# Kernel tuning notes

Hardware: AMD Instinct MI355X
Metric: run time of the kernel (lower is better)

Reference implementation:

```python
import jax, jax.numpy as jnp
import numpy as np

EMBED_DIM = 1024
NUM_HEADS = 16
HEAD_DIM = EMBED_DIM // NUM_HEADS
SCALE = float(np.sqrt(HEAD_DIM))


def setup_inputs() -> dict:
    key = jax.random.key(0)
    ks = jax.random.split(key, 5)
    B, S, D = 4, 2048, EMBED_DIM
    lim_qkv = 1.0 / np.sqrt(D)
    lim_out = 1.0 / np.sqrt(D)
    return {
        "x": jax.random.normal(ks[0], (B, S, D), dtype=jnp.float32),
        "qkv_w": jax.random.uniform(ks[1], (3 * D, D), jnp.float32, -lim_qkv, lim_qkv),
        "qkv_b": jax.random.uniform(ks[2], (3 * D,), jnp.float32, -lim_qkv, lim_qkv),
        "out_w": jax.random.uniform(ks[3], (D, D), jnp.float32, -lim_out, lim_out),
        "out_b": jax.random.uniform(ks[4], (D,), jnp.float32, -lim_out, lim_out),
    }


def reference(x, qkv_w, qkv_b, out_w, out_b):
    B, S, D = x.shape
    H, Hd = NUM_HEADS, HEAD_DIM
    # qkv projection (torch Linear: x @ W.T + b)
    qkv = x @ qkv_w.T + qkv_b                      # [B, S, 3D]
    qkv = qkv.reshape(B, S, 3, H, Hd)
    q = jnp.transpose(qkv[:, :, 0], (0, 2, 1, 3))  # [B, H, S, Hd]
    k = jnp.transpose(qkv[:, :, 1], (0, 2, 1, 3))
    v = jnp.transpose(qkv[:, :, 2], (0, 2, 1, 3))
    attn = jnp.einsum("bhqd,bhkd->bhqk", q, k) / SCALE  # [B, H, S, S]
    attn = jax.nn.softmax(attn, axis=-1)
    out = jnp.einsum("bhqk,bhkd->bhqd", attn, v)        # [B, H, S, Hd]
    out = jnp.transpose(out, (0, 2, 1, 3)).reshape(B, S, D)
    return out @ out_w.T + out_b
```

## Files before the change

### kernel.cpp

```cpp
#include <hip/hip_runtime.h>

typedef unsigned short u16;
typedef __bf16 bf16x8 __attribute__((ext_vector_type(8)));
typedef __bf16 bf16x4 __attribute__((ext_vector_type(4)));
typedef float f32x4 __attribute__((ext_vector_type(4)));
typedef float f32x16 __attribute__((ext_vector_type(16)));
typedef unsigned u32x2 __attribute__((ext_vector_type(2)));

#define AS1 __attribute__((address_space(1)))
#define AS3 __attribute__((address_space(3)))

__device__ __forceinline__ void gload_lds16(const void* g, void* l) {
  __builtin_amdgcn_global_load_lds((const AS1 void*)g, (AS3 void*)l, 16, 0, 0);
}

__device__ __forceinline__ f32x4 mfma16(bf16x8 a, bf16x8 b, f32x4 c) {
  return __builtin_amdgcn_mfma_f32_16x16x32_bf16(a, b, c, 0, 0, 0);
}
__device__ __forceinline__ f32x16 mfma32(bf16x8 a, bf16x8 b, f32x16 c) {
  return __builtin_amdgcn_mfma_f32_32x32x16_bf16(a, b, c, 0, 0, 0);
}

#define QSCALE 0.18033688011112042f

__global__ __launch_bounds__(256) void k_cvt3(const float* __restrict__ s0, u16* __restrict__ d0, int n0,
                                              const float* __restrict__ s1, u16* __restrict__ d1, int n1,
                                              const float* __restrict__ s2, u16* __restrict__ d2, int n2) {
  int g = (blockIdx.x * 256 + threadIdx.x) * 8;
  const float* src;
  u16* dst;
  int i;
  if (g < n0) { src = s0; dst = d0; i = g; }
  else if (g < n0 + n1) { src = s1; dst = d1; i = g - n0; }
  else if (g < n0 + n1 + n2) { src = s2; dst = d2; i = g - n0 - n1; }
  else return;
  float4 a = *(const float4*)(src + i);
  float4 b = *(const float4*)(src + i + 4);
  union { bf16x8 v; uint4 q; } o;
  o.v[0] = (__bf16)a.x; o.v[1] = (__bf16)a.y; o.v[2] = (__bf16)a.z; o.v[3] = (__bf16)a.w;
  o.v[4] = (__bf16)b.x; o.v[5] = (__bf16)b.y; o.v[6] = (__bf16)b.z; o.v[7] = (__bf16)b.w;
  *(uint4*)(dst + i) = o.q;
}

template <int MODE, int BXN>
__global__ __launch_bounds__(512, 2) void k_gemm_big(
    const u16* __restrict__ A, const u16* __restrict__ W,
    const float* __restrict__ bias, float* __restrict__ Cout,
    u16* __restrict__ Qo, u16* __restrict__ Ko, u16* __restrict__ Vo) {
  __shared__ __align__(16) u16 LDS[2][6 * 4096];

  const int t = threadIdx.x;
  const int lane = t & 63;
  const int w = t >> 6;
  const int wm = w >> 1;
  const int wn = w & 1;
  const int lr = lane & 15;
  const int hi = lane >> 4;

  const int TOT = BXN * 32;
  const int flat = blockIdx.x;
  const int nb = (flat & 7) * (TOT >> 3) + (flat >> 3);
  const int by = nb / BXN;
  const int bx = nb - by * BXN;
  const int m0 = by * 256;
  const int n0 = bx * 128;

  const int tt = t & 255;
  const int g = t >> 8;
  const int tu = (tt & 15) ^ (tt >> 4);
  const int sro = (tu >> 3) * 32 + (tt >> 4);
  const int scol = (tu & 7) * 8;

  auto STAGE = [&](int buf, int kt, int pLo, int pHi) {
    for (int p = pLo; p < pHi; ++p) {
      int st = p * 2 + g;
      const u16* base = (st < 4) ? (A + (size_t)(m0 + st * 64) * 1024)
                                 : (W + (size_t)(n0 + (st - 4) * 64) * 1024);
#pragma unroll
      for (int i = 0; i < 2; ++i)
        gload_lds16(base + (size_t)(sro + i * 16) * 1024 + kt * 64 + scol,
                    &LDS[buf][st * 4096 + i * 2048 + tt * 8]);
    }
  };

  f32x4 acc[4][4] = {};

  STAGE(0, 0, 0, 3);

  for (int kt = 0; kt < 16; ++kt) {
    const int cur = kt & 1;
    asm volatile("s_waitcnt vmcnt(0)" ::: "memory");
    __builtin_amdgcn_sched_barrier(0);
    __builtin_amdgcn_s_barrier();
    __builtin_amdgcn_sched_barrier(0);

    const u16* ab = &LDS[cur][wm * 4096];
    const u16* bb = &LDS[cur][(4 + wn) * 4096];

#pragma unroll
    for (int ks = 0; ks < 2; ++ks) {
      bf16x8 af[4], bfr[4];
#pragma unroll
      for (int mi = 0; mi < 4; ++mi)
        af[mi] = *(const bf16x8*)(ab + ((mi & 1) * 16 + lr) * 128 +
                                  (((ks * 4 + hi + 8 * (mi >> 1)) ^ lr) << 3));
#pragma unroll
      for (int ni = 0; ni < 4; ++ni)
        bfr[ni] = *(const bf16x8*)(bb + ((ni & 1) * 16 + lr) * 128 +
                                   (((ks * 4 + hi + 8 * (ni >> 1)) ^ lr) << 3));
      if (kt + 1 < 16) STAGE(cur ^ 1, kt + 1, ks ? 2 : 0, ks ? 3 : 2);
      asm volatile("s_waitcnt lgkmcnt(0)" ::: "memory");
      __builtin_amdgcn_sched_barrier(0);
      __builtin_amdgcn_s_setprio(1);
#pragma unroll
      for (int mi = 0; mi < 4; ++mi)
#pragma unroll
        for (int ni = 0; ni < 4; ++ni)
          acc[mi][ni] = mfma16(bfr[ni], af[mi], acc[mi][ni]);
      __builtin_amdgcn_s_setprio(0);
      __builtin_amdgcn_sched_barrier(0);
      if (ks == 0) __builtin_amdgcn_s_barrier();
    }
  }

  f32x4 bv[4];
#pragma unroll
  for (int ni = 0; ni < 4; ++ni)
    bv[ni] = *(const f32x4*)(bias + n0 + wn * 64 + ni * 16 + hi * 4);

  if (MODE == 0) {
    const int N = BXN * 128;
#pragma unroll
    for (int mi = 0; mi < 4; ++mi) {
      const int m = m0 + wm * 64 + mi * 16 + lr;
#pragma unroll
      for (int ni = 0; ni < 4; ++ni) {
        f32x4 o = acc[mi][ni] + bv[ni];
        *(f32x4*)(Cout + (size_t)m * N + n0 + wn * 64 + ni * 16 + hi * 4) = o;
      }
    }
  } else {
    const int bb16 = m0 >> 11;
    const int sb = (m0 & 2047) + wm * 64;
    const int which = n0 >> 10;
    const int h = ((n0 & 1023) >> 6) + wn;

    if (which < 2) {
      const float scl = (which == 0) ? QSCALE : 1.0f;
      u16* dst = ((which == 0) ? Qo : Ko) + ((size_t)(bb16 * 16 + h) * 2048) * 64;
#pragma unroll
      for (int mi = 0; mi < 4; ++mi) {
        const int s = sb + mi * 16 + lr;
#pragma unroll
        for (int ni = 0; ni < 4; ++ni) {
          bf16x4 pk;
#pragma unroll
          for (int j = 0; j < 4; ++j)
            pk[j] = (__bf16)((acc[mi][ni][j] + bv[ni][j]) * scl);
          *(bf16x4*)(dst + (size_t)s * 64 + ni * 16 + hi * 4) = pk;
        }
      }
    } else {
      __syncthreads();
      u16* scr = &LDS[0][0] + w * 4608;
#pragma unroll
      for (int mi = 0; mi < 4; ++mi)
#pragma unroll
        for (int ni = 0; ni < 4; ++ni)
#pragma unroll
          for (int j = 0; j < 4; ++j) {
            union { __bf16 b; u16 u; } cv;
            cv.b = (__bf16)(acc[mi][ni][j] + bv[ni][j]);
            scr[(ni * 16 + hi * 4 + j) * 72 + mi * 16 + lr] = cv.u;
          }
      asm volatile("s_waitcnt lgkmcnt(0)" ::: "memory");
      __builtin_amdgcn_sched_barrier(0);
      u16* dst = Vo + ((size_t)((bb16 * 16 + h) * 64 + lane)) * 2048 + sb;
#pragma unroll
      for (int mc = 0; mc < 8; ++mc) {
        bf16x8 vv = *(const bf16x8*)(scr + lane * 72 + mc * 8);
        *(bf16x8*)(dst + mc * 8) = vv;
      }
    }
  }
}

__global__ __launch_bounds__(256, 4) void k_attn(const u16* __restrict__ Q,
                                                 const u16* __restrict__ K,
                                                 const u16* __restrict__ Vt,
                                                 u16* __restrict__ ctx) {
  __shared__ __align__(16) u16 Ks[2][64 * 64];
  __shared__ __align__(16) u16 Vs[2][64 * 64];

  const int t = threadIdx.x;
  const int lane = t & 63;
  const int w = t >> 6;
  const int r31 = lane & 31;
  const int hw = lane >> 5;

  const int bid = blockIdx.x;
  const int nb = (bid & 7) * 128 + (bid >> 3);
  const int bh = nb >> 4;
  const int q0 = (nb & 15) * 128;

  const u16* qp = Q + (size_t)bh * 2048 * 64;
  const u16* kp = K + (size_t)bh * 2048 * 64;
  const u16* vp = Vt + (size_t)bh * 64 * 2048;

  const int tu = (t & 15) ^ (t >> 4);
  const int srow = (tu >> 3) * 32 + (t >> 4);
  const int scol = (tu & 7) * 8;

#pragma unroll
  for (int i = 0; i < 2; i++)
    gload_lds16(kp + (size_t)(srow + i * 16) * 64 + scol, Ks[0] + i * 2048 + t * 8);
#pragma unroll
  for (int i = 0; i < 2; i++)
    gload_lds16(vp + (size_t)(srow + i * 16) * 2048 + scol, Vs[0] + i * 2048 + t * 8);

  bf16x8 aq[4];
  const u16* qrow = qp + (size_t)(q0 + w * 32 + r31) * 64 + hw * 8;
#pragma unroll
  for (int kd = 0; kd < 4; kd++) aq[kd] = *(const bf16x8*)(qrow + kd * 16);

  bf16x8 ones;
#pragma unroll
  for (int e = 0; e < 8; e++) ones[e] = (__bf16)1.0f;

  asm volatile("s_waitcnt vmcnt(0)" ::: "memory");
  __builtin_amdgcn_sched_barrier(0);
  __builtin_amdgcn_s_barrier();
  __builtin_amdgcn_sched_barrier(0);

  f32x16 o0 = {}, o1 = {}, l_acc = {};

  for (int kt = 0; kt < 32; kt++) {
    const int cur = kt & 1;
    if (kt + 1 < 32) {
      u16* kd_ = Ks[cur ^ 1];
      u16* vd_ = Vs[cur ^ 1];
#pragma unroll
      for (int i = 0; i < 2; i++)
        gload_lds16(kp + (size_t)((kt + 1) * 64 + srow + i * 16) * 64 + scol,
                    kd_ + i * 2048 + t * 8);
#pragma unroll
      for (int i = 0; i < 2; i++)
        gload_lds16(vp + (size_t)(srow + i * 16) * 2048 + (kt + 1) * 64 + scol,
                    vd_ + i * 2048 + t * 8);
      asm volatile("s_waitcnt vmcnt(4)" ::: "memory");
    } else {
      asm volatile("s_waitcnt vmcnt(0)" ::: "memory");
    }
    __builtin_amdgcn_sched_barrier(0);
    __builtin_amdgcn_s_barrier();
    __builtin_amdgcn_sched_barrier(0);

    const u16* kb = Ks[cur];
    const u16* vb = Vs[cur];

    f32x16 s0 = {}, s1 = {};
    __builtin_amdgcn_s_setprio(1);
#pragma unroll
    for (int kd = 0; kd < 4; kd++) {
      int sl0 = (((kd * 2 + hw) ^ (r31 & 15)) << 3);
      int sl1 = (((8 + kd * 2 + hw) ^ (r31 & 15)) << 3);
      bf16x8 ka0 = *(const bf16x8*)(kb + r31 * 128 + sl0);
      bf16x8 ka1 = *(const bf16x8*)(kb + r31 * 128 + sl1);
      s0 = mfma32(ka0, aq[kd], s0);
      s1 = mfma32(ka1, aq[kd], s1);
    }
    __builtin_amdgcn_s_setprio(0);

#pragma unroll
    for (int e = 0; e < 16; e++) {
      s0[e] = __builtin_amdgcn_exp2f(s0[e]);
      s1[e] = __builtin_amdgcn_exp2f(s1[e]);
    }

    __builtin_amdgcn_s_setprio(1);
#pragma unroll
    for (int tile = 0; tile < 2; tile++) {
      f32x16 st = tile ? s1 : s0;
      unsigned pk[8];
#pragma unroll
      for (int p = 0; p < 8; p++) {
        union { __bf16 h[2]; unsigned u; } cv;
        cv.h[0] = (__bf16)st[2 * p];
        cv.h[1] = (__bf16)st[2 * p + 1];
        pk[p] = cv.u;
      }
#pragma unroll
      for (int c = 0; c < 2; c++) {
        u32x2 ra = __builtin_amdgcn_permlane32_swap(pk[4 * c], pk[4 * c + 2], false, false);
        u32x2 rb = __builtin_amdgcn_permlane32_swap(pk[4 * c + 1], pk[4 * c + 3], false, false);
        union { unsigned u[4]; bf16x8 v; } pf;
        pf.u[0] = ra[0]; pf.u[1] = rb[0]; pf.u[2] = ra[1]; pf.u[3] = rb[1];
        const int kap = tile * 2 + c;
        int slv0 = (((kap * 2 + hw) ^ (r31 & 15)) << 3);
        int slv1 = (((8 + kap * 2 + hw) ^ (r31 & 15)) << 3);
        bf16x8 v0 = *(const bf16x8*)(vb + r31 * 128 + slv0);
        bf16x8 v1 = *(const bf16x8*)(vb + r31 * 128 + slv1);
        o0 = mfma32(v0, pf.v, o0);
        o1 = mfma32(v1, pf.v, o1);
        l_acc = mfma32(ones, pf.v, l_acc);
      }
    }
    __builtin_amdgcn_s_setprio(0);
    __builtin_amdgcn_sched_barrier(0);
    __builtin_amdgcn_s_barrier();
  }

  const int bb = bh >> 4, h = bh & 15;
  const float inv = 1.0f / l_acc[0];
  const size_t base = (size_t)(bb * 2048 + q0 + w * 32 + r31) * 1024 + h * 64;
#pragma unroll
  for (int g = 0; g < 4; g++) {
    bf16x4 p0, p1;
#pragma unroll
    for (int j = 0; j < 4; j++) {
      p0[j] = (__bf16)(o0[g * 4 + j] * inv);
      p1[j] = (__bf16)(o1[g * 4 + j] * inv);
    }
    *(bf16x4*)(ctx + base + g * 8 + hw * 4) = p0;
    *(bf16x4*)(ctx + base + 32 + g * 8 + hw * 4) = p1;
  }
}

extern "C" void kernel_launch(void* const* d_in, const int* in_sizes, int n_in,
                              void* d_out, int out_size, void* d_ws, size_t ws_size,
                              hipStream_t stream) {
  const float* x = (const float*)d_in[0];
  const float* qkv_w = (const float*)d_in[1];
  const float* qkv_b = (const float*)d_in[2];
  const float* out_w = (const float*)d_in[3];
  const float* out_b = (const float*)d_in[4];
  float* out = (float*)d_out;
  char* ws = (char*)d_ws;

  u16* xb    = (u16*)(ws + 0);
  u16* wqkvb = (u16*)(ws + 16777216);
  u16* wob   = (u16*)(ws + 23068672);
  u16* Qb    = (u16*)(ws + 25165824);
  u16* Kb    = (u16*)(ws + 41943040);
  u16* Vtb   = (u16*)(ws + 58720256);
  u16* ctx   = xb;

  k_cvt3<<<6144, 256, 0, stream>>>(x, xb, 8388608,
                                   qkv_w, wqkvb, 3145728,
                                   out_w, wob, 1048576);

  k_gemm_big<1, 24><<<768, 512, 0, stream>>>(xb, wqkvb, qkv_b, nullptr,
                                             Qb, Kb, Vtb);
  k_attn<<<1024, 256, 0, stream>>>(Qb, Kb, Vtb, ctx);
  k_gemm_big<0, 8><<<256, 512, 0, stream>>>(ctx, wob, out_b, out,
                                            nullptr, nullptr, nullptr);
}
```

Measured before the change: 198.6 us.

## Stagger KV tile order per block and use single barrier per iteration

Each block starts its key/value loop at a different tile offset (phase), so concurrently running blocks on the same head read different K/V tiles. The loop is restructured to wait on all outstanding loads and take one barrier at the top, then issue the next tile's prefetch, which drops the second barrier at the loop end. The first QK MFMA uses a constant zero accumulator instead of zero-initialised registers. The prefetch now overlaps only the current tile's compute rather than being issued ahead of the wait, and the fixed 32-tile wraparound assumes the sequence length.

After: 197.4 us. Within noise of the previous version (-0.6%).

```diff
diff --git a/kernel.cpp b/kernel.cpp
--- a/kernel.cpp
+++ b/kernel.cpp
@@ -202,6 +202,7 @@
   const int nb = (bid & 7) * 128 + (bid >> 3);
   const int bh = nb >> 4;
   const int q0 = (nb & 15) * 128;
+  const int phase = (((bid >> 8) ^ (bid >> 3)) & 3) * 8;
 
   const u16* qp = Q + (size_t)bh * 2048 * 64;
   const u16* kp = K + (size_t)bh * 2048 * 64;
@@ -213,10 +214,12 @@
 
 #pragma unroll
   for (int i = 0; i < 2; i++)
-    gload_lds16(kp + (size_t)(srow + i * 16) * 64 + scol, Ks[0] + i * 2048 + t * 8);
+    gload_lds16(kp + (size_t)(phase * 64 + srow + i * 16) * 64 + scol,
+                Ks[0] + i * 2048 + t * 8);
 #pragma unroll
   for (int i = 0; i < 2; i++)
-    gload_lds16(vp + (size_t)(srow + i * 16) * 2048 + scol, Vs[0] + i * 2048 + t * 8);
+    gload_lds16(vp + (size_t)(srow + i * 16) * 2048 + phase * 64 + scol,
+                Vs[0] + i * 2048 + t * 8);
 
   bf16x8 aq[4];
   const u16* qrow = qp + (size_t)(q0 + w * 32 + r31) * 64 + hw * 8;
@@ -226,42 +229,44 @@
   bf16x8 ones;
 #pragma unroll
   for (int e = 0; e < 8; e++) ones[e] = (__bf16)1.0f;
-
-  asm volatile("s_waitcnt vmcnt(0)" ::: "memory");
-  __builtin_amdgcn_sched_barrier(0);
-  __builtin_amdgcn_s_barrier();
-  __builtin_amdgcn_sched_barrier(0);
+  const f32x16 Z = {};
 
   f32x16 o0 = {}, o1 = {}, l_acc = {};
 
-  for (int kt = 0; kt < 32; kt++) {
-    const int cur = kt & 1;
-    if (kt + 1 < 32) {
-      u16* kd_ = Ks[cur ^ 1];
-      u16* vd_ = Vs[cur ^ 1];
-#pragma unroll
-      for (int i = 0; i < 2; i++)
-        gload_lds16(kp + (size_t)((kt + 1) * 64 + srow + i * 16) * 64 + scol,
-                    kd_ + i * 2048 + t * 8);
-#pragma unroll
-      for (int i = 0; i < 2; i++)
-        gload_lds16(vp + (size_t)(srow + i * 16) * 2048 + (kt + 1) * 64 + scol,
-                    vd_ + i * 2048 + t * 8);
-      asm volatile("s_waitcnt vmcnt(4)" ::: "memory");
-    } else {
-      asm volatile("s_waitcnt vmcnt(0)" ::: "memory");
-    }
+  for (int it = 0; it < 32; it++) {
+    const int cur = it & 1;
+    asm volatile("s_waitcnt vmcnt(0)" ::: "memory");
     __builtin_amdgcn_sched_barrier(0);
     __builtin_amdgcn_s_barrier();
     __builtin_amdgcn_sched_barrier(0);
 
+    if (it + 1 < 32) {
+      const int ktn = ((it + 1 + phase) & 31) * 64;
+      u16* kd_ = Ks[cur ^ 1];
+      u16* vd_ = Vs[cur ^ 1];
+#pragma unroll
+      for (int i = 0; i < 2; i++)
+        gload_lds16(kp + (size_t)(ktn + srow + i * 16) * 64 + scol,
+                    kd_ + i * 2048 + t * 8);
+#pragma unroll
+      for (int i = 0; i < 2; i++)
+        gload_lds16(vp + (size_t)(srow + i * 16) * 2048 + ktn + scol,
+                    vd_ + i * 2048 + t * 8);
+    }
+
     const u16* kb = Ks[cur];
     const u16* vb = Vs[cur];
 
-    f32x16 s0 = {}, s1 = {};
     __builtin_amdgcn_s_setprio(1);
-#pragma unroll
-    for (int kd = 0; kd < 4; kd++) {
+    f32x16 s0, s1;
+    {
+      bf16x8 ka0 = *(const bf16x8*)(kb + r31 * 128 + (((hw) ^ (r31 & 15)) << 3));
+      bf16x8 ka1 = *(const bf16x8*)(kb + r31 * 128 + (((8 + hw) ^ (r31 & 15)) << 3));
+      s0 = mfma32(ka0, aq[0], Z);
+      s1 = mfma32(ka1, aq[0], Z);
+    }
+#pragma unroll
+    for (int kd = 1; kd < 4; kd++) {
       int sl0 = (((kd * 2 + hw) ^ (r31 & 15)) << 3);
       int sl1 = (((8 + kd * 2 + hw) ^ (r31 & 15)) << 3);
       bf16x8 ka0 = *(const bf16x8*)(kb + r31 * 128 + sl0);
@@ -306,8 +311,6 @@
       }
     }
     __builtin_amdgcn_s_setprio(0);
-    __builtin_amdgcn_sched_barrier(0);
-    __builtin_amdgcn_s_barrier();
   }
 
   const int bb = bh >> 4, h = bh & 15;
```

## Software-pipeline attention loop: overlap QK/exp of next tile with PV of current

Applied to the files above, without the earlier changes.

Restructures the attention inner loop so the QK^T, exp and packing for key tile k+1 run in the same step as the P·V MMAs for tile k, with K and V staged into LDS at offset iterations. The row-sum is now computed with scalar adds and a cross-half shuffle instead of an extra MFMA against a ones vector. This aims to hide exp/pack latency behind matrix work and cut MFMA count, in exchange for more live registers and a full vmcnt(0) wait each sub-step.

Result: slower. 368.6 us (+85.6%).

```diff
diff --git a/kernel.cpp b/kernel.cpp
--- a/kernel.cpp
+++ b/kernel.cpp
@@ -19,6 +19,33 @@
 }
 __device__ __forceinline__ f32x16 mfma32(bf16x8 a, bf16x8 b, f32x16 c) {
   return __builtin_amdgcn_mfma_f32_32x32x16_bf16(a, b, c, 0, 0, 0);
+}
+
+__device__ __forceinline__ float rsum16(f32x16 v) {
+  float a0 = v[0] + v[1],  a1 = v[2] + v[3];
+  float a2 = v[4] + v[5],  a3 = v[6] + v[7];
+  float a4 = v[8] + v[9],  a5 = v[10] + v[11];
+  float a6 = v[12] + v[13], a7 = v[14] + v[15];
+  return ((a0 + a1) + (a2 + a3)) + ((a4 + a5) + (a6 + a7));
+}
+
+__device__ __forceinline__ void pack2(const f32x16& st, bf16x8& f0, bf16x8& f1) {
+  unsigned pk[8];
+#pragma unroll
+  for (int p = 0; p < 8; p++) {
+    union { __bf16 h[2]; unsigned u; } cv;
+    cv.h[0] = (__bf16)st[2 * p];
+    cv.h[1] = (__bf16)st[2 * p + 1];
+    pk[p] = cv.u;
+  }
+  u32x2 ra = __builtin_amdgcn_permlane32_swap(pk[0], pk[2], false, false);
+  u32x2 rb = __builtin_amdgcn_permlane32_swap(pk[1], pk[3], false, false);
+  u32x2 rc = __builtin_amdgcn_permlane32_swap(pk[4], pk[6], false, false);
+  u32x2 rd = __builtin_amdgcn_permlane32_swap(pk[5], pk[7], false, false);
+  union { unsigned u[4]; bf16x8 v; } a, b;
+  a.u[0] = ra[0]; a.u[1] = rb[0]; a.u[2] = ra[1]; a.u[3] = rb[1];
+  b.u[0] = rc[0]; b.u[1] = rd[0]; b.u[2] = rc[1]; b.u[3] = rd[1];
+  f0 = a.v; f1 = b.v;
 }
 
 #define QSCALE 0.18033688011112042f
@@ -211,107 +238,96 @@
   const int srow = (tu >> 3) * 32 + (t >> 4);
   const int scol = (tu & 7) * 8;
 
-#pragma unroll
-  for (int i = 0; i < 2; i++)
-    gload_lds16(kp + (size_t)(srow + i * 16) * 64 + scol, Ks[0] + i * 2048 + t * 8);
-#pragma unroll
-  for (int i = 0; i < 2; i++)
-    gload_lds16(vp + (size_t)(srow + i * 16) * 2048 + scol, Vs[0] + i * 2048 + t * 8);
+  auto stageK = [&](int kt, u16* dst) {
+#pragma unroll
+    for (int i = 0; i < 2; i++)
+      gload_lds16(kp + (size_t)(kt * 64 + srow + i * 16) * 64 + scol,
+                  dst + i * 2048 + t * 8);
+  };
+  auto stageV = [&](int kt, u16* dst) {
+#pragma unroll
+    for (int i = 0; i < 2; i++)
+      gload_lds16(vp + (size_t)(srow + i * 16) * 2048 + kt * 64 + scol,
+                  dst + i * 2048 + t * 8);
+  };
 
   bf16x8 aq[4];
   const u16* qrow = qp + (size_t)(q0 + w * 32 + r31) * 64 + hw * 8;
 #pragma unroll
   for (int kd = 0; kd < 4; kd++) aq[kd] = *(const bf16x8*)(qrow + kd * 16);
 
-  bf16x8 ones;
-#pragma unroll
-  for (int e = 0; e < 8; e++) ones[e] = (__bf16)1.0f;
-
+  const f32x16 Z = {};
+  f32x16 o0 = {}, o1 = {};
+  float l = 0.f;
+  bf16x8 pfA[4], pfB[4];
+
+  auto HALF = [&](const u16* kb, int base, bf16x8& f0, bf16x8& f1) -> float {
+    f32x16 s;
+    {
+      bf16x8 ka = *(const bf16x8*)(kb + r31 * 128 + (((base + hw) ^ (r31 & 15)) << 3));
+      s = mfma32(ka, aq[0], Z);
+    }
+#pragma unroll
+    for (int kd = 1; kd < 4; kd++) {
+      bf16x8 ka = *(const bf16x8*)(kb + r31 * 128 + (((base + kd * 2 + hw) ^ (r31 & 15)) << 3));
+      s = mfma32(ka, aq[kd], s);
+    }
+#pragma unroll
+    for (int e = 0; e < 16; e++) s[e] = __builtin_amdgcn_exp2f(s[e]);
+    pack2(s, f0, f1);
+    return rsum16(s);
+  };
+
+  auto PV = [&](const u16* vb, bf16x8 (&pf)[4]) {
+    __builtin_amdgcn_s_setprio(1);
+#pragma unroll
+    for (int kap = 0; kap < 4; kap++) {
+      bf16x8 v0 = *(const bf16x8*)(vb + r31 * 128 + (((kap * 2 + hw) ^ (r31 & 15)) << 3));
+      bf16x8 v1 = *(const bf16x8*)(vb + r31 * 128 + (((8 + kap * 2 + hw) ^ (r31 & 15)) << 3));
+      o0 = mfma32(v0, pf[kap], o0);
+      o1 = mfma32(v1, pf[kap], o1);
+    }
+    __builtin_amdgcn_s_setprio(0);
+  };
+
+  stageK(0, Ks[0]);
+  stageK(1, Ks[1]);
+  stageV(0, Vs[0]);
   asm volatile("s_waitcnt vmcnt(0)" ::: "memory");
   __builtin_amdgcn_sched_barrier(0);
   __builtin_amdgcn_s_barrier();
   __builtin_amdgcn_sched_barrier(0);
-
-  f32x16 o0 = {}, o1 = {}, l_acc = {};
-
-  for (int kt = 0; kt < 32; kt++) {
-    const int cur = kt & 1;
-    if (kt + 1 < 32) {
-      u16* kd_ = Ks[cur ^ 1];
-      u16* vd_ = Vs[cur ^ 1];
-#pragma unroll
-      for (int i = 0; i < 2; i++)
-        gload_lds16(kp + (size_t)((kt + 1) * 64 + srow + i * 16) * 64 + scol,
-                    kd_ + i * 2048 + t * 8);
-#pragma unroll
-      for (int i = 0; i < 2; i++)
-        gload_lds16(vp + (size_t)(srow + i * 16) * 2048 + (kt + 1) * 64 + scol,
-                    vd_ + i * 2048 + t * 8);
-      asm volatile("s_waitcnt vmcnt(4)" ::: "memory");
-    } else {
-      asm volatile("s_waitcnt vmcnt(0)" ::: "memory");
-    }
+  {
+    float rs = HALF(Ks[0], 0, pfA[0], pfA[1]);
+    rs += HALF(Ks[0], 8, pfA[2], pfA[3]);
+    rs += __shfl_xor(rs, 32);
+    l += rs;
+  }
+
+  auto SUB = [&](int kS, u16* kD, int vS, u16* vD, const u16* kR, const u16* vR,
+                 bf16x8 (&pfUse)[4], bf16x8 (&pfMake)[4], bool doQ) {
+    asm volatile("s_waitcnt vmcnt(0)" ::: "memory");
     __builtin_amdgcn_sched_barrier(0);
     __builtin_amdgcn_s_barrier();
     __builtin_amdgcn_sched_barrier(0);
-
-    const u16* kb = Ks[cur];
-    const u16* vb = Vs[cur];
-
-    f32x16 s0 = {}, s1 = {};
-    __builtin_amdgcn_s_setprio(1);
-#pragma unroll
-    for (int kd = 0; kd < 4; kd++) {
-      int sl0 = (((kd * 2 + hw) ^ (r31 & 15)) << 3);
-      int sl1 = (((8 + kd * 2 + hw) ^ (r31 & 15)) << 3);
-      bf16x8 ka0 = *(const bf16x8*)(kb + r31 * 128 + sl0);
-      bf16x8 ka1 = *(const bf16x8*)(kb + r31 * 128 + sl1);
-      s0 = mfma32(ka0, aq[kd], s0);
-      s1 = mfma32(ka1, aq[kd], s1);
-    }
-    __builtin_amdgcn_s_setprio(0);
-
-#pragma unroll
-    for (int e = 0; e < 16; e++) {
-      s0[e] = __builtin_amdgcn_exp2f(s0[e]);
-      s1[e] = __builtin_amdgcn_exp2f(s1[e]);
-    }
-
-    __builtin_amdgcn_s_setprio(1);
-#pragma unroll
-    for (int tile = 0; tile < 2; tile++) {
-      f32x16 st = tile ? s1 : s0;
-      unsigned pk[8];
-#pragma unroll
-      for (int p = 0; p < 8; p++) {
-        union { __bf16 h[2]; unsigned u; } cv;
-        cv.h[0] = (__bf16)st[2 * p];
-        cv.h[1] = (__bf16)st[2 * p + 1];
-        pk[p] = cv.u;
-      }
-#pragma unroll
-      for (int c = 0; c < 2; c++) {
-        u32x2 ra = __builtin_amdgcn_permlane32_swap(pk[4 * c], pk[4 * c + 2], false, false);
-        u32x2 rb = __builtin_amdgcn_permlane32_swap(pk[4 * c + 1], pk[4 * c + 3], false, false);
-        union { unsigned u[4]; bf16x8 v; } pf;
-        pf.u[0] = ra[0]; pf.u[1] = rb[0]; pf.u[2] = ra[1]; pf.u[3] = rb[1];
-        const int kap = tile * 2 + c;
-        int slv0 = (((kap * 2 + hw) ^ (r31 & 15)) << 3);
-        int slv1 = (((8 + kap * 2 + hw) ^ (r31 & 15)) << 3);
-        bf16x8 v0 = *(const bf16x8*)(vb + r31 * 128 + slv0);
-        bf16x8 v1 = *(const bf16x8*)(vb + r31 * 128 + slv1);
-        o0 = mfma32(v0, pf.v, o0);
-        o1 = mfma32(v1, pf.v, o1);
-        l_acc = mfma32(ones, pf.v, l_acc);
-      }
-    }
-    __builtin_amdgcn_s_setprio(0);
-    __builtin_amdgcn_sched_barrier(0);
-    __builtin_amdgcn_s_barrier();
+    if (kS < 32) stageK(kS, kD);
+    if (vS < 32) stageV(vS, vD);
+    if (doQ) {
+      float rs = HALF(kR, 0, pfMake[0], pfMake[1]);
+      rs += HALF(kR, 8, pfMake[2], pfMake[3]);
+      rs += __shfl_xor(rs, 32);
+      l += rs;
+    }
+    PV(vR, pfUse);
+  };
+
+  for (int k = 0; k < 16; ++k) {
+    SUB(2 * k + 2, Ks[0], 2 * k + 1, Vs[1], Ks[1], Vs[0], pfA, pfB, true);
+    SUB(2 * k + 3, Ks[1], 2 * k + 2, Vs[0], Ks[0], Vs[1], pfB, pfA, k < 15);
   }
 
   const int bb = bh >> 4, h = bh & 15;
-  const float inv = 1.0f / l_acc[0];
+  const float inv = 1.0f / l;
   const size_t base = (size_t)(bb * 2048 + q0 + w * 32 + r31) * 1024 + h * 64;
 #pragma unroll
   for (int g = 0; g < 4; g++) {
```
